# Kernel tuning notes

Measured on AMD Instinct MI355X. Metric: run time of the kernel, lower is better.

The kernel has to match this reference:

```python
import jax, jax.numpy as jnp
import numpy as np

N_NODES = 100000
IN_F = 256
OUT_F = 128
N_EDGES = 1600000


def setup_inputs() -> dict:
    key = jax.random.key(0)
    k1, k2, k3, k4 = jax.random.split(key, 4)
    inputs = jax.random.normal(k1, (N_NODES, IN_F), dtype=jnp.float32)
    edge = jax.random.randint(k2, (2, N_EDGES), 0, N_NODES, dtype=jnp.int64)
    # xavier_uniform for weight [in, out]
    bw = float(np.sqrt(6.0 / (IN_F + OUT_F)))
    weight = jax.random.uniform(k3, (IN_F, OUT_F), minval=-bw, maxval=bw, dtype=jnp.float32)
    ba = float(np.sqrt(6.0 / (OUT_F + 1)))
    a = jax.random.uniform(k4, (OUT_F, 1), minval=-ba, maxval=ba, dtype=jnp.float32)
    return {"inputs": inputs, "edge": edge, "weight": weight, "a": a}


def reference(inputs, edge, weight, a):
    # h: [N, out_features]
    h = inputs @ weight
    # edge-wise gather + abs-diff: [E, out_features]
    diff = jnp.abs(h[edge[0]] - h[edge[1]])
    # dot with attention vector a, relu, squeeze -> [E]
    edge_weight = jax.nn.relu((diff @ a).squeeze(-1))
    return (h, edge_weight)
```

## Files before the change

kernel.cpp:

```cpp
#include <hip/hip_runtime.h>
#include <hip/hip_bf16.h>
#include <stdint.h>

typedef __bf16 bf16x8 __attribute__((ext_vector_type(8)));
typedef float  f32x4  __attribute__((ext_vector_type(4)));

#define M_NODES 100000
#define K_IN    256
#define N_OUT   128
#define N_EDGE  1600000

__global__ __launch_bounds__(256) void gemm_h_mfma(
    const float* __restrict__ in,
    const float* __restrict__ w,
    float* __restrict__ h,
    __hip_bfloat16* __restrict__ hmir)
{
    const int lane = threadIdx.x & 63;
    const int wave = threadIdx.x >> 6;
    const int m0   = blockIdx.x * 64;
    const int nb   = wave * 32;

    const int lr = lane & 15;
    const int q  = lane >> 4;

    f32x4 acc[4][2];
    #pragma unroll
    for (int mt = 0; mt < 4; ++mt)
        #pragma unroll
        for (int nt = 0; nt < 2; ++nt)
            acc[mt][nt] = f32x4{0.f, 0.f, 0.f, 0.f};

    for (int kk = 0; kk < K_IN; kk += 32) {
        const int ka = kk + q * 8;

        bf16x8 afrag[4];
        #pragma unroll
        for (int mt = 0; mt < 4; ++mt) {
            const int row = m0 + mt * 16 + lr;
            if (row < M_NODES) {
                const float* ap = in + (size_t)row * K_IN + ka;
                const f32x4 a0 = *(const f32x4*)ap;
                const f32x4 a1 = *(const f32x4*)(ap + 4);
                #pragma unroll
                for (int j = 0; j < 4; ++j) {
                    afrag[mt][j]     = (__bf16)a0[j];
                    afrag[mt][4 + j] = (__bf16)a1[j];
                }
            } else {
                #pragma unroll
                for (int j = 0; j < 8; ++j) afrag[mt][j] = (__bf16)0.f;
            }
        }

        bf16x8 bfrag[2];
        #pragma unroll
        for (int nt = 0; nt < 2; ++nt) {
            const int col = nb + nt * 16 + lr;
            #pragma unroll
            for (int j = 0; j < 8; ++j)
                bfrag[nt][j] = (__bf16)w[(size_t)(ka + j) * N_OUT + col];
        }

        #pragma unroll
        for (int mt = 0; mt < 4; ++mt)
            #pragma unroll
            for (int nt = 0; nt < 2; ++nt)
                acc[mt][nt] = __builtin_amdgcn_mfma_f32_16x16x32_bf16(
                    afrag[mt], bfrag[nt], acc[mt][nt], 0, 0, 0);
    }

    #pragma unroll
    for (int mt = 0; mt < 4; ++mt) {
        const int rb = m0 + mt * 16 + q * 4;
        if (rb >= M_NODES) continue;
        #pragma unroll
        for (int nt = 0; nt < 2; ++nt) {
            const int col = nb + nt * 16 + lr;
            #pragma unroll
            for (int r = 0; r < 4; ++r) {
                const float v = acc[mt][nt][r];
                __builtin_nontemporal_store(v, h + (size_t)(rb + r) * N_OUT + col);
                hmir[(size_t)(rb + r) * N_OUT + col] = __float2bfloat16(v);
            }
        }
    }
}

__device__ inline int detect_i64(const uint32_t* p) {
    return __popcll(__ballot(p[2 * (threadIdx.x & 63) + 1] == 0u)) >= 60;
}

__global__ __launch_bounds__(256) void edge_kernel_bf16(
    const __hip_bfloat16* __restrict__ hm,
    const uint32_t* __restrict__ edge_raw,
    const float* __restrict__ a,
    float* __restrict__ ew,
    int E)
{
    const int e64 = detect_i64(edge_raw);
    const int s = threadIdx.x & 15;
    const int e = (int)((blockIdx.x * 256 + threadIdx.x) >> 4);
    if (e >= E) return;

    int src, dst;
    if (e64) {
        src = (int)edge_raw[2 * (size_t)e];
        dst = (int)edge_raw[2 * ((size_t)E + e)];
    } else {
        const int* e32 = (const int*)edge_raw;
        src = e32[e];
        dst = e32[(size_t)E + e];
    }

    const __bf16* hb = (const __bf16*)hm;
    const bf16x8 hs = *(const bf16x8*)(hb + (size_t)src * N_OUT + s * 8);
    const bf16x8 hd = *(const bf16x8*)(hb + (size_t)dst * N_OUT + s * 8);
    const f32x4 a0 = *(const f32x4*)(a + s * 8);
    const f32x4 a1 = *(const f32x4*)(a + s * 8 + 4);

    float sum = 0.f;
    #pragma unroll
    for (int i = 0; i < 4; ++i)
        sum += fabsf((float)hs[i] - (float)hd[i]) * a0[i];
    #pragma unroll
    for (int i = 0; i < 4; ++i)
        sum += fabsf((float)hs[4 + i] - (float)hd[4 + i]) * a1[i];

    sum += __shfl_xor(sum, 1, 64);
    sum += __shfl_xor(sum, 2, 64);
    sum += __shfl_xor(sum, 4, 64);
    sum += __shfl_xor(sum, 8, 64);

    if (s == 0) ew[e] = fmaxf(sum, 0.f);
}

__global__ __launch_bounds__(256) void edge_kernel_f32(
    const float* __restrict__ h,
    const uint32_t* __restrict__ edge_raw,
    const float* __restrict__ a,
    float* __restrict__ ew,
    int E)
{
    const int e64 = detect_i64(edge_raw);
    const int s = threadIdx.x & 15;
    const int e = (int)((blockIdx.x * 256 + threadIdx.x) >> 4);
    if (e >= E) return;

    int src, dst;
    if (e64) {
        src = (int)edge_raw[2 * (size_t)e];
        dst = (int)edge_raw[2 * ((size_t)E + e)];
    } else {
        const int* e32 = (const int*)edge_raw;
        src = e32[e];
        dst = e32[(size_t)E + e];
    }

    const f32x4 s0 = *(const f32x4*)(h + (size_t)src * N_OUT + s * 8);
    const f32x4 s1 = *(const f32x4*)(h + (size_t)src * N_OUT + s * 8 + 4);
    const f32x4 d0 = *(const f32x4*)(h + (size_t)dst * N_OUT + s * 8);
    const f32x4 d1 = *(const f32x4*)(h + (size_t)dst * N_OUT + s * 8 + 4);
    const f32x4 a0 = *(const f32x4*)(a + s * 8);
    const f32x4 a1 = *(const f32x4*)(a + s * 8 + 4);

    float sum = 0.f;
    #pragma unroll
    for (int i = 0; i < 4; ++i) sum += fabsf(s0[i] - d0[i]) * a0[i];
    #pragma unroll
    for (int i = 0; i < 4; ++i) sum += fabsf(s1[i] - d1[i]) * a1[i];

    sum += __shfl_xor(sum, 1, 64);
    sum += __shfl_xor(sum, 2, 64);
    sum += __shfl_xor(sum, 4, 64);
    sum += __shfl_xor(sum, 8, 64);

    if (s == 0) ew[e] = fmaxf(sum, 0.f);
}

extern "C" void kernel_launch(void* const* d_in, const int* in_sizes, int n_in,
                              void* d_out, int out_size, void* d_ws, size_t ws_size,
                              hipStream_t stream) {
    const float*    in   = (const float*)d_in[0];
    const uint32_t* edge = (const uint32_t*)d_in[1];
    const float*    w    = (const float*)d_in[2];
    const float*    a    = (const float*)d_in[3];

    float* h  = (float*)d_out;
    float* ew = h + (size_t)M_NODES * N_OUT;

    const size_t mirror_bytes = (size_t)M_NODES * N_OUT * sizeof(__hip_bfloat16);
    __hip_bfloat16* hmir =
        (ws_size >= mirror_bytes) ? (__hip_bfloat16*)d_ws : nullptr;

    if (hmir) {
        gemm_h_mfma<<<dim3((M_NODES + 63) / 64), dim3(256), 0, stream>>>(
            in, w, h, hmir);
        const int eblocks = (N_EDGE * 16 + 255) / 256;
        edge_kernel_bf16<<<dim3(eblocks), dim3(256), 0, stream>>>(
            hmir, edge, a, ew, N_EDGE);
    } else {
        gemm_h_mfma<<<dim3((M_NODES + 63) / 64), dim3(256), 0, stream>>>(
            in, w, h, (__hip_bfloat16*)d_ws);
        const int eblocks = (N_EDGE * 16 + 255) / 256;
        edge_kernel_f32<<<dim3(eblocks), dim3(256), 0, stream>>>(
            h, edge, a, ew, N_EDGE);
    }
}
```

Before: 327.8 us.

## Persistent GEMM with register-resident weights and 4-edge-per-group edge kernel

```diff
diff --git a/kernel.cpp b/kernel.cpp
--- a/kernel.cpp
+++ b/kernel.cpp
@@ -10,20 +10,13 @@
 #define N_OUT   128
 #define N_EDGE  1600000
 
-__global__ __launch_bounds__(256) void gemm_h_mfma(
-    const float* __restrict__ in,
-    const float* __restrict__ w,
-    float* __restrict__ h,
-    __hip_bfloat16* __restrict__ hmir)
-{
-    const int lane = threadIdx.x & 63;
-    const int wave = threadIdx.x >> 6;
-    const int m0   = blockIdx.x * 64;
-    const int nb   = wave * 32;
-
-    const int lr = lane & 15;
-    const int q  = lane >> 4;
-
+template <bool FULL>
+__device__ __forceinline__ void gemm_tile(
+    const float* __restrict__ in, float* __restrict__ h,
+    __hip_bfloat16* __restrict__ hmir,
+    const bf16x8 (&bfrag)[8][2], const int m0, const int lr, const int q,
+    const int nb)
+{
     f32x4 acc[4][2];
     #pragma unroll
     for (int mt = 0; mt < 4; ++mt)
@@ -31,14 +24,14 @@
         for (int nt = 0; nt < 2; ++nt)
             acc[mt][nt] = f32x4{0.f, 0.f, 0.f, 0.f};
 
-    for (int kk = 0; kk < K_IN; kk += 32) {
-        const int ka = kk + q * 8;
-
+    #pragma unroll
+    for (int k8 = 0; k8 < 8; ++k8) {
+        const int ka = k8 * 32 + q * 8;
         bf16x8 afrag[4];
         #pragma unroll
         for (int mt = 0; mt < 4; ++mt) {
             const int row = m0 + mt * 16 + lr;
-            if (row < M_NODES) {
+            if (FULL || row < M_NODES) {
                 const float* ap = in + (size_t)row * K_IN + ka;
                 const f32x4 a0 = *(const f32x4*)ap;
                 const f32x4 a1 = *(const f32x4*)(ap + 4);
@@ -52,28 +45,18 @@
                 for (int j = 0; j < 8; ++j) afrag[mt][j] = (__bf16)0.f;
             }
         }
-
-        bf16x8 bfrag[2];
-        #pragma unroll
-        for (int nt = 0; nt < 2; ++nt) {
-            const int col = nb + nt * 16 + lr;
-            #pragma unroll
-            for (int j = 0; j < 8; ++j)
-                bfrag[nt][j] = (__bf16)w[(size_t)(ka + j) * N_OUT + col];
-        }
-
         #pragma unroll
         for (int mt = 0; mt < 4; ++mt)
             #pragma unroll
             for (int nt = 0; nt < 2; ++nt)
                 acc[mt][nt] = __builtin_amdgcn_mfma_f32_16x16x32_bf16(
-                    afrag[mt], bfrag[nt], acc[mt][nt], 0, 0, 0);
+                    afrag[mt], bfrag[k8][nt], acc[mt][nt], 0, 0, 0);
     }
 
     #pragma unroll
     for (int mt = 0; mt < 4; ++mt) {
         const int rb = m0 + mt * 16 + q * 4;
-        if (rb >= M_NODES) continue;
+        if (!FULL && rb >= M_NODES) continue;
         #pragma unroll
         for (int nt = 0; nt < 2; ++nt) {
             const int col = nb + nt * 16 + lr;
@@ -87,12 +70,134 @@
     }
 }
 
+__global__ __launch_bounds__(256) void gemm_h_mfma(
+    const float* __restrict__ in,
+    const float* __restrict__ w,
+    float* __restrict__ h,
+    __hip_bfloat16* __restrict__ hmir)
+{
+    const int lane = threadIdx.x & 63;
+    const int wave = threadIdx.x >> 6;
+    const int nb   = wave * 32;
+    const int lr   = lane & 15;
+    const int q    = lane >> 4;
+
+    bf16x8 bfrag[8][2];
+    #pragma unroll
+    for (int k8 = 0; k8 < 8; ++k8) {
+        const int ka = k8 * 32 + q * 8;
+        #pragma unroll
+        for (int nt = 0; nt < 2; ++nt) {
+            const int col = nb + nt * 16 + lr;
+            #pragma unroll
+            for (int j = 0; j < 8; ++j)
+                bfrag[k8][nt][j] = (__bf16)w[(size_t)(ka + j) * N_OUT + col];
+        }
+    }
+
+    const int ntiles = (M_NODES + 63) / 64;
+    const int nfull  = M_NODES / 64;
+    for (int t = blockIdx.x; t < ntiles; t += gridDim.x) {
+        const int m0 = t * 64;
+        if (t < nfull) gemm_tile<true >(in, h, hmir, bfrag, m0, lr, q, nb);
+        else           gemm_tile<false>(in, h, hmir, bfrag, m0, lr, q, nb);
+    }
+}
+
 __device__ inline int detect_i64(const uint32_t* p) {
     return __popcll(__ballot(p[2 * (threadIdx.x & 63) + 1] == 0u)) >= 60;
 }
 
 __global__ __launch_bounds__(256) void edge_kernel_bf16(
     const __hip_bfloat16* __restrict__ hm,
+    const uint32_t* __restrict__ edge_raw,
+    const float* __restrict__ a,
+    float* __restrict__ ew,
+    int E)
+{
+    const int e64 = detect_i64(edge_raw);
+    const int s  = threadIdx.x & 15;
+    const int g  = (int)((blockIdx.x * 256 + threadIdx.x) >> 4);
+    const int e0 = g * 4;
+    if (e0 >= E) return;
+
+    const __bf16* hb = (const __bf16*)hm;
+    const f32x4 a0 = *(const f32x4*)(a + s * 8);
+    const f32x4 a1 = *(const f32x4*)(a + s * 8 + 4);
+
+    if (e0 + 3 < E) {
+        int srcs[4], dsts[4];
+        if (e64) {
+            const uint4 s01 = *(const uint4*)(edge_raw + 2 * (size_t)e0);
+            const uint4 s23 = *(const uint4*)(edge_raw + 2 * (size_t)e0 + 4);
+            const uint4 d01 = *(const uint4*)(edge_raw + 2 * ((size_t)E + e0));
+            const uint4 d23 = *(const uint4*)(edge_raw + 2 * ((size_t)E + e0) + 4);
+            srcs[0] = (int)s01.x; srcs[1] = (int)s01.z;
+            srcs[2] = (int)s23.x; srcs[3] = (int)s23.z;
+            dsts[0] = (int)d01.x; dsts[1] = (int)d01.z;
+            dsts[2] = (int)d23.x; dsts[3] = (int)d23.z;
+        } else {
+            const int4 sv = *(const int4*)((const int*)edge_raw + e0);
+            const int4 dv = *(const int4*)((const int*)edge_raw + (size_t)E + e0);
+            srcs[0] = sv.x; srcs[1] = sv.y; srcs[2] = sv.z; srcs[3] = sv.w;
+            dsts[0] = dv.x; dsts[1] = dv.y; dsts[2] = dv.z; dsts[3] = dv.w;
+        }
+
+        bf16x8 hs[4], hd[4];
+        #pragma unroll
+        for (int u = 0; u < 4; ++u) {
+            hs[u] = *(const bf16x8*)(hb + (size_t)srcs[u] * N_OUT + s * 8);
+            hd[u] = *(const bf16x8*)(hb + (size_t)dsts[u] * N_OUT + s * 8);
+        }
+
+        f32x4 r;
+        #pragma unroll
+        for (int u = 0; u < 4; ++u) {
+            float sum = 0.f;
+            #pragma unroll
+            for (int i = 0; i < 4; ++i)
+                sum += fabsf((float)hs[u][i] - (float)hd[u][i]) * a0[i];
+            #pragma unroll
+            for (int i = 0; i < 4; ++i)
+                sum += fabsf((float)hs[u][4 + i] - (float)hd[u][4 + i]) * a1[i];
+            sum += __shfl_xor(sum, 1, 64);
+            sum += __shfl_xor(sum, 2, 64);
+            sum += __shfl_xor(sum, 4, 64);
+            sum += __shfl_xor(sum, 8, 64);
+            r[u] = fmaxf(sum, 0.f);
+        }
+        if (s == 0) *(f32x4*)(ew + e0) = r;
+    } else {
+        for (int e = e0; e < E; ++e) {
+            int src, dst;
+            if (e64) {
+                src = (int)edge_raw[2 * (size_t)e];
+                dst = (int)edge_raw[2 * ((size_t)E + e)];
+            } else {
+                const int* e32 = (const int*)edge_raw;
+                src = e32[e];
+                dst = e32[(size_t)E + e];
+            }
+            const bf16x8 hs = *(const bf16x8*)(hb + (size_t)src * N_OUT + s * 8);
+            const bf16x8 hd = *(const bf16x8*)(hb + (size_t)dst * N_OUT + s * 8);
+            float sum = 0.f;
+            #pragma unroll
+            for (int i = 0; i < 4; ++i)
+                sum += fabsf((float)hs[i] - (float)hd[i]) * a0[i];
+            #pragma unroll
+            for (int i = 0; i < 4; ++i)
+                sum += fabsf((float)hs[4 + i] - (float)hd[4 + i]) * a1[i];
+            sum += __shfl_xor(sum, 1, 64);
+            sum += __shfl_xor(sum, 2, 64);
+            sum += __shfl_xor(sum, 4, 64);
+            sum += __shfl_xor(sum, 8, 64);
+            if (s == 0) ew[e] = fmaxf(sum, 0.f);
+        }
+    }
+}
+
+__global__ __launch_bounds__(256) void edge_kernel_f32(
+    const float* __restrict__ h,
     const uint32_t* __restrict__ edge_raw,
     const float* __restrict__ a,
     float* __restrict__ ew,
@@ -113,50 +218,6 @@
         dst = e32[(size_t)E + e];
     }
 
-    const __bf16* hb = (const __bf16*)hm;
-    const bf16x8 hs = *(const bf16x8*)(hb + (size_t)src * N_OUT + s * 8);
-    const bf16x8 hd = *(const bf16x8*)(hb + (size_t)dst * N_OUT + s * 8);
-    const f32x4 a0 = *(const f32x4*)(a + s * 8);
-    const f32x4 a1 = *(const f32x4*)(a + s * 8 + 4);
-
-    float sum = 0.f;
-    #pragma unroll
-    for (int i = 0; i < 4; ++i)
-        sum += fabsf((float)hs[i] - (float)hd[i]) * a0[i];
-    #pragma unroll
-    for (int i = 0; i < 4; ++i)
-        sum += fabsf((float)hs[4 + i] - (float)hd[4 + i]) * a1[i];
-
-    sum += __shfl_xor(sum, 1, 64);
-    sum += __shfl_xor(sum, 2, 64);
-    sum += __shfl_xor(sum, 4, 64);
-    sum += __shfl_xor(sum, 8, 64);
-
-    if (s == 0) ew[e] = fmaxf(sum, 0.f);
-}
-
-__global__ __launch_bounds__(256) void edge_kernel_f32(
-    const float* __restrict__ h,
-    const uint32_t* __restrict__ edge_raw,
-    const float* __restrict__ a,
-    float* __restrict__ ew,
-    int E)
-{
-    const int e64 = detect_i64(edge_raw);
-    const int s = threadIdx.x & 15;
-    const int e = (int)((blockIdx.x * 256 + threadIdx.x) >> 4);
-    if (e >= E) return;
-
-    int src, dst;
-    if (e64) {
-        src = (int)edge_raw[2 * (size_t)e];
-        dst = (int)edge_raw[2 * ((size_t)E + e)];
-    } else {
-        const int* e32 = (const int*)edge_raw;
-        src = e32[e];
-        dst = e32[(size_t)E + e];
-    }
-
     const f32x4 s0 = *(const f32x4*)(h + (size_t)src * N_OUT + s * 8);
     const f32x4 s1 = *(const f32x4*)(h + (size_t)src * N_OUT + s * 8 + 4);
     const f32x4 d0 = *(const f32x4*)(h + (size_t)dst * N_OUT + s * 8);
@@ -194,13 +255,13 @@
         (ws_size >= mirror_bytes) ? (__hip_bfloat16*)d_ws : nullptr;
 
     if (hmir) {
-        gemm_h_mfma<<<dim3((M_NODES + 63) / 64), dim3(256), 0, stream>>>(
-            in, w, h, hmir);
-        const int eblocks = (N_EDGE * 16 + 255) / 256;
+        gemm_h_mfma<<<dim3(512), dim3(256), 0, stream>>>(in, w, h, hmir);
+        const int egroups = (N_EDGE + 3) / 4;
+        const int eblocks = (egroups * 16 + 255) / 256;
         edge_kernel_bf16<<<dim3(eblocks), dim3(256), 0, stream>>>(
             hmir, edge, a, ew, N_EDGE);
     } else {
-        gemm_h_mfma<<<dim3((M_NODES + 63) / 64), dim3(256), 0, stream>>>(
+        gemm_h_mfma<<<dim3(512), dim3(256), 0, stream>>>(
             in, w, h, (__hip_bfloat16*)d_ws);
         const int eblocks = (N_EDGE * 16 + 255) / 256;
         edge_kernel_f32<<<dim3(eblocks), dim3(256), 0, stream>>>(
```

Result: faster. 298.6 us (-8.9%).
